# Performance work log

Hardware: AMD Instinct MI355X
Metric: run time of the kernel (lower is better)

Reference implementation:

```python
import jax, jax.numpy as jnp
import numpy as np

IN, H, OUT = 1536, 640, 10
BATCH = 65536
KEEP = 0.1


def setup_inputs() -> dict:
    key = jax.random.key(0)
    kx, k1, k2, k3, m1, m2, m3 = jax.random.split(key, 7)
    # torch.nn.Linear-style weights: (out_features, in_features)
    W1 = jax.random.normal(k1, (H, IN), dtype=jnp.float32) * (1.0 / np.sqrt(IN))
    W2 = jax.random.normal(k2, (H, H), dtype=jnp.float32) * (1.0 / np.sqrt(H))
    W3 = jax.random.normal(k3, (OUT, H), dtype=jnp.float32) * (1.0 / np.sqrt(H))
    return {
        "x": jax.random.normal(kx, (BATCH, IN), dtype=jnp.float32),
        "W1": W1,
        "W2": W2,
        "W3": W3,
        "mask1": jax.random.bernoulli(m1, KEEP, (H, IN)),
        "mask2": jax.random.bernoulli(m2, KEEP, (H, H)),
        "mask3": jax.random.bernoulli(m3, KEEP, (OUT, H)),
    }


def reference(x, W1, W2, W3, mask1, mask2, mask3):
    w1 = jnp.where(mask1, W1, 0.0)
    w2 = jnp.where(mask2, W2, 0.0)
    w3 = jnp.where(mask3, W3, 0.0)
    h = jax.nn.gelu(x @ w1.T, approximate=False)       # [B, 640], exact GELU like F.gelu
    h = jax.nn.gelu(h @ w2.T, approximate=False)       # [B, 640]
    return h @ w3.T                                    # [B, 10]
```

## Files before the change

### kernel.cpp

```cpp
#include <hip/hip_runtime.h>
#include <hip/hip_fp16.h>
#include <math.h>

typedef _Float16 half_t;
typedef __attribute__((ext_vector_type(8))) _Float16 f16x8;
typedef __attribute__((ext_vector_type(4))) float   f32x4;
typedef __attribute__((ext_vector_type(4))) float   float4v;

#define IN_F   1536
#define HID    640
#define OUT_F  10
#define NBATCH 65536

#define SB() __builtin_amdgcn_sched_barrier(0)


__device__ __forceinline__ void gll16(const void* g, const void* l) {
    __builtin_amdgcn_global_load_lds(
        (const __attribute__((address_space(1))) unsigned*)g,
        (__attribute__((address_space(3))) unsigned*)l, 16, 0, 0);
}

__device__ __forceinline__ float gelu_fast(float z) {
    float x  = 0.70710678118654752f * z;
    float ax = fabsf(x);
    float t  = 1.0f / (1.0f + 0.3275911f * ax);
    float p  = t * (0.254829592f +
               t * (-0.284496736f +
               t * (1.421413741f +
               t * (-1.453152027f +
               t * 1.061405429f))));
    float e  = __expf(-ax * ax);
    float er = 1.0f - p * e;
    er = (x < 0.0f) ? -er : er;
    return 0.5f * z * (1.0f + er);
}


__global__ void k_detect(const unsigned* __restrict__ m, int nDwords, int* flags) {
    int f = 0, g = 0;
    for (int i = blockIdx.x * blockDim.x + threadIdx.x; i < nDwords;
         i += gridDim.x * blockDim.x) {
        unsigned d = m[i];
        f |= (d == 0x3F800000u);
        g |= (d != 0u) & (d != 1u) & (d != 0x3F800000u);
    }
    if (f) atomicOr(&flags[0], 1);
    if (g) atomicOr(&flags[1], 1);
}

__device__ __forceinline__ bool mask_at(const void* mask, int i, int isB, int isF) {
    if (isB) return ((const unsigned char*)mask)[i] != 0;
    if (isF) return ((const float*)mask)[i] != 0.0f;
    return ((const int*)mask)[i] != 0;
}

__global__ void k_mask_all(const float* __restrict__ W1, const float* __restrict__ W2,
                           const float* __restrict__ W3,
                           const void* __restrict__ m1, const void* __restrict__ m2,
                           const void* __restrict__ m3,
                           half_t* __restrict__ W1h, half_t* __restrict__ W2h,
                           float* __restrict__ W3m, const int* __restrict__ flags) {
    const int isB = flags[1], isF = flags[0];
    const int N1 = HID * IN_F, N2 = HID * HID, N3 = OUT_F * HID;
    const int NT = N1 + N2 + N3;
    for (int i = blockIdx.x * blockDim.x + threadIdx.x; i < NT;
         i += gridDim.x * blockDim.x) {
        if (i < N1) {
            W1h[i] = mask_at(m1, i, isB, isF) ? (half_t)W1[i] : (half_t)0.0f;
        } else if (i < N1 + N2) {
            int j = i - N1;
            W2h[j] = mask_at(m2, j, isB, isF) ? (half_t)W2[j] : (half_t)0.0f;
        } else {
            int j = i - N1 - N2;
            W3m[j] = mask_at(m3, j, isB, isF) ? W3[j] : 0.0f;
        }
    }
}

__global__ __launch_bounds__(256, 3) void gemm1_tall(
    const float* __restrict__ Ain, const half_t* __restrict__ Bw,
    half_t* __restrict__ Cout) {
    constexpr int K    = IN_F;
    constexpr int NK   = K / 32;
    constexpr int SLAB = 16384 + 10240;
    __shared__ __align__(16) char lds[2 * SLAB];

    const int t = threadIdx.x, lane = t & 63, wid = t >> 6;
    const int wr = wid >> 1, wc = wid & 1;

    const int q       = (int)gridDim.x >> 3;
    const int logical = ((int)blockIdx.x & 7) * q + ((int)blockIdx.x >> 3);
    const int mb = logical >> 2, nbk = logical & 3;
    const long mBase = (long)mb * 128;
    const int  n0    = nbk * 160;

    const int rr = lane & 15, k8 = lane >> 4;

    int aRd[4], bRd[5];
    {
#pragma unroll
        for (int mf = 0; mf < 4; ++mf) {
            const int row = wr * 64 + mf * 16 + rr;
            aRd[mf] = row * 128 + (((2 * k8) ^ (row & 7)) << 4);
        }
#pragma unroll
        for (int nf = 0; nf < 5; ++nf) {
            const int nrow = wc * 80 + nf * 16 + rr, ln = nrow >> 1;
            bRd[nf] = 16384 + ln * 128 +
                      ((((((nrow & 1) << 2) | k8)) ^ (ln & 7)) << 4);
        }
    }

    const float* srcAf;
    {
        const int row = t >> 3, kq = (t & 7) ^ ((t >> 3) & 7);
        srcAf = Ain + (mBase + row) * (long)K + kq * 4;
    }
    const half_t* srcB;
    {
        const int line = t >> 3, orig = (t & 7) ^ (line & 7);
        const int nrow = 2 * line + (orig >> 2), kq = orig & 3;
        srcB = Bw + (size_t)(n0 + nrow) * K + kq * 8;
    }

    auto STAGE = [&](int k, int sb) {
        const size_t ko = (size_t)k * 32;
#pragma unroll
        for (int r = 0; r < 4; ++r)
            gll16(srcAf + ko + (size_t)r * 32 * K,
                  &lds[sb + (t + r * 256) * 16]);
#pragma unroll
        for (int r = 0; r < 2; ++r)
            gll16(srcB + ko + (size_t)r * 64 * K,
                  &lds[sb + 16384 + (t + r * 256) * 16]);
        if (t < 128)
            gll16(srcB + ko + (size_t)128 * K,
                  &lds[sb + 16384 + (t + 512) * 16]);
    };

    f32x4 acc[4][5];
#pragma unroll
    for (int mf = 0; mf < 4; ++mf)
#pragma unroll
        for (int nf = 0; nf < 5; ++nf) {
            f32x4 z = {0.f, 0.f, 0.f, 0.f};
            acc[mf][nf] = z;
        }

    STAGE(0, 0); SB();
    STAGE(1, SLAB); SB();

    for (int ks = 0; ks < NK; ++ks) {
        const int cb = (ks & 1) * SLAB;
        if (ks + 1 < NK) {
            if (wid < 2) asm volatile("s_waitcnt vmcnt(7)" ::: "memory");
            else         asm volatile("s_waitcnt vmcnt(6)" ::: "memory");
        } else {
            asm volatile("s_waitcnt vmcnt(0)" ::: "memory");
        }
        __builtin_amdgcn_s_barrier();
        f16x8 bv[5];
#pragma unroll
        for (int nf = 0; nf < 5; ++nf)
            bv[nf] = *(const f16x8*)(&lds[cb + bRd[nf]]);
        f16x8 av[4];
#pragma unroll
        for (int mf = 0; mf < 4; ++mf) {
            float4v alo = *(const float4v*)(&lds[cb + aRd[mf]]);
            float4v ahi = *(const float4v*)(&lds[cb + (aRd[mf] ^ 16)]);
            f16x8 h;
#pragma unroll
            for (int i = 0; i < 4; ++i) {
                h[i]     = (half_t)alo[i];
                h[i + 4] = (half_t)ahi[i];
            }
            av[mf] = h;
        }
        asm volatile("s_waitcnt lgkmcnt(0)" ::: "memory");
        SB();
        __builtin_amdgcn_s_barrier();
        if (ks + 2 < NK) { STAGE(ks + 2, cb); SB(); }
#pragma unroll
        for (int mf = 0; mf < 4; ++mf)
#pragma unroll
            for (int nf = 0; nf < 5; ++nf)
                acc[mf][nf] = __builtin_amdgcn_mfma_f32_16x16x32_f16(
                    av[mf], bv[nf], acc[mf][nf], 0, 0, 0);
    }

    const int crow0 = (lane >> 4) * 4;
    const int ccol  = lane & 15;
#pragma unroll
    for (int mf = 0; mf < 4; ++mf)
#pragma unroll
        for (int nf = 0; nf < 5; ++nf)
#pragma unroll
            for (int j = 0; j < 4; ++j) {
                const long row = mBase + wr * 64 + mf * 16 + crow0 + j;
                const int  col = n0 + wc * 80 + nf * 16 + ccol;
                Cout[row * HID + col] = (half_t)gelu_fast(acc[mf][nf][j]);
            }
}

template <int K>
__global__ __launch_bounds__(512, 2) void gemm2_fused(
    const half_t* __restrict__ Ain, const half_t* __restrict__ Bw,
    const float* __restrict__ W3, float* __restrict__ Pout) {
    constexpr int NK     = K / 32;
    constexpr int ABYTES = 16384;
    constexpr int SLAB   = ABYTES + 20480;
    __shared__ __align__(16) char lds[3 * SLAB];

    const int t = threadIdx.x, lane = t & 63, wid = t >> 6;
    const int wr = wid >> 2, wc = wid & 3;

    const int q       = (int)gridDim.x >> 3;
    const int logical = ((int)blockIdx.x & 7) * q + ((int)blockIdx.x >> 3);
    const int mb = logical >> 1, nbk = logical & 1;
    const long mBase = (long)mb * 256;
    const int  n0    = nbk * 320;

    const int rr = lane & 15, k8 = lane >> 4;

    int aBase0 = 0, bBase = 0;
    {
        const int row = wr * 128 + rr, ln = row >> 1;
        aBase0 = ln * 128 + ((((((row & 1) << 2) | k8)) ^ (ln & 7)) << 4);
        const int nrow = wc * 80 + rr, lnb = nrow >> 1;
        bBase = ABYTES + lnb * 128 +
                ((((((nrow & 1) << 2) | k8)) ^ (lnb & 7)) << 4);
    }

    const half_t* srcAh;
    {
        const int line = t >> 3, orig = (t & 7) ^ (line & 7);
        const int row = 2 * line + (orig >> 2), kq = orig & 3;
        srcAh = Ain + (mBase + row) * (long)K + kq * 8;
    }
    const half_t* srcB;
    {
        const int line = t >> 3, orig = (t & 7) ^ (line & 7);
        const int nrow = 2 * line + (orig >> 2), kq = orig & 3;
        srcB = Bw + (size_t)(n0 + nrow) * K + kq * 8;
    }

    auto STAGE = [&](int k, int sb) {
        const size_t ko = (size_t)k * 32;
#pragma unroll
        for (int r = 0; r < 2; ++r)
            gll16(srcAh + ko + (size_t)r * 128 * K,
                  &lds[sb + (t + r * 512) * 16]);
#pragma unroll
        for (int r = 0; r < 2; ++r)
            gll16(srcB + ko + (size_t)r * 128 * K,
                  &lds[sb + ABYTES + (t + r * 512) * 16]);
        if (t < 256)
            gll16(srcB + ko + (size_t)2 * 128 * K,
                  &lds[sb + ABYTES + (t + 1024) * 16]);
    };

    f32x4 acc[8][5];
#pragma unroll
    for (int mf = 0; mf < 8; ++mf)
#pragma unroll
        for (int nf = 0; nf < 5; ++nf) {
            f32x4 z = {0.f, 0.f, 0.f, 0.f};
            acc[mf][nf] = z;
        }

    STAGE(0, 0); SB();
    STAGE(1, SLAB); SB();

    for (int ks = 0; ks < NK; ++ks) {
        if (ks + 1 < NK) {
            if (wid < 4) asm volatile("s_waitcnt vmcnt(5)" ::: "memory");
            else         asm volatile("s_waitcnt vmcnt(4)" ::: "memory");
        } else {
            asm volatile("s_waitcnt vmcnt(0)" ::: "memory");
        }
        __builtin_amdgcn_s_barrier();
        const int cb = (ks % 3) * SLAB;
        if (ks + 2 < NK) { STAGE(ks + 2, ((ks + 2) % 3) * SLAB); SB(); }

        f16x8 bv[5];
#pragma unroll
        for (int nf = 0; nf < 5; ++nf)
            bv[nf] = *(const f16x8*)(&lds[cb + bBase + nf * 1024]);
        f16x8 av[8];
#pragma unroll
        for (int mf = 0; mf < 8; ++mf)
            av[mf] = *(const f16x8*)(&lds[cb + aBase0 + mf * 1024]);
#pragma unroll
        for (int mf = 0; mf < 8; ++mf)
#pragma unroll
            for (int nf = 0; nf < 5; ++nf)
                acc[mf][nf] = __builtin_amdgcn_mfma_f32_16x16x32_f16(
                    av[mf], bv[nf], acc[mf][nf], 0, 0, 0);
    }

    const int crow0 = (lane >> 4) * 4;
    const int ccol  = lane & 15;
    float w3[OUT_F][5];
#pragma unroll
    for (int o = 0; o < OUT_F; ++o)
#pragma unroll
        for (int nf = 0; nf < 5; ++nf)
            w3[o][nf] = W3[o * HID + n0 + wc * 80 + nf * 16 + ccol];
    float* slice = Pout + (size_t)(nbk * 4 + wc) * NBATCH * OUT_F;
#pragma unroll
    for (int mf = 0; mf < 8; ++mf)
#pragma unroll
        for (int j = 0; j < 4; ++j) {
            float p[OUT_F];
#pragma unroll
            for (int o = 0; o < OUT_F; ++o) p[o] = 0.f;
#pragma unroll
            for (int nf = 0; nf < 5; ++nf) {
                const float v = gelu_fast(acc[mf][nf][j]);
#pragma unroll
                for (int o = 0; o < OUT_F; ++o) p[o] += v * w3[o][nf];
            }
#pragma unroll
            for (int mask = 1; mask < 16; mask <<= 1)
#pragma unroll
                for (int o = 0; o < OUT_F; ++o)
                    p[o] += __shfl_xor(p[o], mask);
            float v = 0.f;
#pragma unroll
            for (int o = 0; o < OUT_F; ++o) v = (ccol == o) ? p[o] : v;
            const long row = mBase + wr * 128 + mf * 16 + crow0 + j;
            if (ccol < OUT_F) slice[row * OUT_F + ccol] = v;
        }
}

__global__ void k_final(const float* __restrict__ P, float* __restrict__ out) {
    const int n = NBATCH * OUT_F;
    for (int i = blockIdx.x * blockDim.x + threadIdx.x; i < n;
         i += gridDim.x * blockDim.x) {
        float s0 = P[i]                 + P[(size_t)1 * n + i];
        float s1 = P[(size_t)2 * n + i] + P[(size_t)3 * n + i];
        float s2 = P[(size_t)4 * n + i] + P[(size_t)5 * n + i];
        float s3 = P[(size_t)6 * n + i] + P[(size_t)7 * n + i];
        out[i] = (s0 + s1) + (s2 + s3);
    }
}


extern "C" void kernel_launch(void* const* d_in, const int* in_sizes, int n_in,
                              void* d_out, int out_size, void* d_ws, size_t ws_size,
                              hipStream_t stream) {
    const float* x  = (const float*)d_in[0];
    const float* W1 = (const float*)d_in[1];
    const float* W2 = (const float*)d_in[2];
    const float* W3 = (const float*)d_in[3];
    const void*  m1 = d_in[4];
    const void*  m2 = d_in[5];
    const void*  m3 = d_in[6];
    float* out = (float*)d_out;

    char* ws = (char*)d_ws;
    int*    flags = (int*)ws;
    half_t* W1h = (half_t*)(ws + 256);
    half_t* W2h = (half_t*)(ws + 256 + 1966080);
    float*  W3m = (float*)(ws + 256 + 1966080 + 819200);
    half_t* h1  = (half_t*)(ws + 256 + 1966080 + 819200 + 25600);
    float*  Pp  = (float*)((char*)h1 + (size_t)NBATCH * HID * 2);

    hipMemsetAsync(flags, 0, 8, stream);
    k_detect<<<64, 256, 0, stream>>>((const unsigned*)m1, 65536, flags);
    k_mask_all<<<1024, 256, 0, stream>>>(W1, W2, W3, m1, m2, m3, W1h, W2h, W3m, flags);

    gemm1_tall<<<2048, 256, 0, stream>>>(x, W1h, h1);
    gemm2_fused<HID><<<512, 512, 0, stream>>>(h1, W2h, W3m, Pp);
    k_final<<<1024, 256, 0, stream>>>(Pp, out);
}
```

Baseline: 357.3 us.

## Enlarge gemm1 tile to 256x320 with triple-buffered, split-stage LDS pipeline

The first GEMM now uses 512-thread blocks, each computing a 256x320 output tile instead of 128x160. Each fp32 activation row is therefore reloaded only twice across the N dimension instead of four times. The K loop moves to a three-slab LDS ring. Staging of the next-but-one slab is split into two halves, interleaved with the two M-half MFMA phases, and those phases run with raised wave priority via s_setprio. The cost is roughly 156 KB of LDS per block, which allows only one block per CU with fewer resident waves, plus more accumulator registers per thread.

```diff
diff --git a/kernel.cpp b/kernel.cpp
--- a/kernel.cpp
+++ b/kernel.cpp
@@ -78,36 +78,36 @@
     }
 }
 
-__global__ __launch_bounds__(256, 3) void gemm1_tall(
+__global__ __launch_bounds__(512, 2) void gemm1_tall(
     const float* __restrict__ Ain, const half_t* __restrict__ Bw,
     half_t* __restrict__ Cout) {
     constexpr int K    = IN_F;
     constexpr int NK   = K / 32;
-    constexpr int SLAB = 16384 + 10240;
-    __shared__ __align__(16) char lds[2 * SLAB];
+    constexpr int SLAB = 32768 + 20480;
+    __shared__ __align__(16) char lds[3 * SLAB];
 
     const int t = threadIdx.x, lane = t & 63, wid = t >> 6;
-    const int wr = wid >> 1, wc = wid & 1;
+    const int wr = wid >> 2, wc = wid & 3;
 
     const int q       = (int)gridDim.x >> 3;
     const int logical = ((int)blockIdx.x & 7) * q + ((int)blockIdx.x >> 3);
-    const int mb = logical >> 2, nbk = logical & 3;
-    const long mBase = (long)mb * 128;
-    const int  n0    = nbk * 160;
+    const int mb = logical >> 1, nbk = logical & 1;
+    const long mBase = (long)mb * 256;
+    const int  n0    = nbk * 320;
 
     const int rr = lane & 15, k8 = lane >> 4;
 
-    int aRd[4], bRd[5];
-    {
-#pragma unroll
-        for (int mf = 0; mf < 4; ++mf) {
-            const int row = wr * 64 + mf * 16 + rr;
+    int aRd[8], bRd[5];
+    {
+#pragma unroll
+        for (int mf = 0; mf < 8; ++mf) {
+            const int row = wr * 128 + mf * 16 + rr;
             aRd[mf] = row * 128 + (((2 * k8) ^ (row & 7)) << 4);
         }
 #pragma unroll
         for (int nf = 0; nf < 5; ++nf) {
             const int nrow = wc * 80 + nf * 16 + rr, ln = nrow >> 1;
-            bRd[nf] = 16384 + ln * 128 +
+            bRd[nf] = 32768 + ln * 128 +
                       ((((((nrow & 1) << 2) | k8)) ^ (ln & 7)) << 4);
         }
     }
@@ -124,80 +124,124 @@
         srcB = Bw + (size_t)(n0 + nrow) * K + kq * 8;
     }
 
-    auto STAGE = [&](int k, int sb) {
+    auto STAGE_A01 = [&](int k, int sb) {
         const size_t ko = (size_t)k * 32;
-#pragma unroll
-        for (int r = 0; r < 4; ++r)
-            gll16(srcAf + ko + (size_t)r * 32 * K,
-                  &lds[sb + (t + r * 256) * 16]);
-#pragma unroll
-        for (int r = 0; r < 2; ++r)
-            gll16(srcB + ko + (size_t)r * 64 * K,
-                  &lds[sb + 16384 + (t + r * 256) * 16]);
-        if (t < 128)
-            gll16(srcB + ko + (size_t)128 * K,
-                  &lds[sb + 16384 + (t + 512) * 16]);
+        gll16(srcAf + ko, &lds[sb + t * 16]);
+        gll16(srcAf + ko + (size_t)64 * K, &lds[sb + (t + 512) * 16]);
     };
-
-    f32x4 acc[4][5];
-#pragma unroll
-    for (int mf = 0; mf < 4; ++mf)
+    auto STAGE_A23_B = [&](int k, int sb) {
+        const size_t ko = (size_t)k * 32;
+        gll16(srcAf + ko + (size_t)128 * K, &lds[sb + (t + 1024) * 16]);
+        gll16(srcAf + ko + (size_t)192 * K, &lds[sb + (t + 1536) * 16]);
+        gll16(srcB + ko,                    &lds[sb + 32768 + t * 16]);
+        gll16(srcB + ko + (size_t)128 * K,  &lds[sb + 32768 + (t + 512) * 16]);
+        if (t < 256)
+            gll16(srcB + ko + (size_t)256 * K,
+                  &lds[sb + 32768 + (t + 1024) * 16]);
+    };
+
+    f32x4 acc[8][5];
+#pragma unroll
+    for (int mf = 0; mf < 8; ++mf)
 #pragma unroll
         for (int nf = 0; nf < 5; ++nf) {
             f32x4 z = {0.f, 0.f, 0.f, 0.f};
             acc[mf][nf] = z;
         }
 
-    STAGE(0, 0); SB();
-    STAGE(1, SLAB); SB();
+    STAGE_A01(0, 0); STAGE_A23_B(0, 0); SB();
+    STAGE_A01(1, SLAB); STAGE_A23_B(1, SLAB); SB();
 
     for (int ks = 0; ks < NK; ++ks) {
-        const int cb = (ks & 1) * SLAB;
+        const int cb  = (ks % 3) * SLAB;
+        const int nsb = ((ks + 2) % 3) * SLAB;
+        const bool st = (ks + 2) < NK;
         if (ks + 1 < NK) {
-            if (wid < 2) asm volatile("s_waitcnt vmcnt(7)" ::: "memory");
+            if (wid < 4) asm volatile("s_waitcnt vmcnt(7)" ::: "memory");
             else         asm volatile("s_waitcnt vmcnt(6)" ::: "memory");
         } else {
             asm volatile("s_waitcnt vmcnt(0)" ::: "memory");
         }
         __builtin_amdgcn_s_barrier();
         f16x8 bv[5];
-#pragma unroll
-        for (int nf = 0; nf < 5; ++nf)
-            bv[nf] = *(const f16x8*)(&lds[cb + bRd[nf]]);
-        f16x8 av[4];
-#pragma unroll
-        for (int mf = 0; mf < 4; ++mf) {
-            float4v alo = *(const float4v*)(&lds[cb + aRd[mf]]);
-            float4v ahi = *(const float4v*)(&lds[cb + (aRd[mf] ^ 16)]);
-            f16x8 h;
-#pragma unroll
-            for (int i = 0; i < 4; ++i) {
-                h[i]     = (half_t)alo[i];
-                h[i + 4] = (half_t)ahi[i];
-            }
-            av[mf] = h;
-        }
-        asm volatile("s_waitcnt lgkmcnt(0)" ::: "memory");
-        SB();
-        __builtin_amdgcn_s_barrier();
-        if (ks + 2 < NK) { STAGE(ks + 2, cb); SB(); }
-#pragma unroll
-        for (int mf = 0; mf < 4; ++mf)
+        {
+            float4v alo[4], ahi[4];
+#pragma unroll
+            for (int m2 = 0; m2 < 4; ++m2) {
+                alo[m2] = *(const float4v*)(&lds[cb + aRd[m2]]);
+                ahi[m2] = *(const float4v*)(&lds[cb + (aRd[m2] ^ 16)]);
+            }
 #pragma unroll
             for (int nf = 0; nf < 5; ++nf)
-                acc[mf][nf] = __builtin_amdgcn_mfma_f32_16x16x32_f16(
-                    av[mf], bv[nf], acc[mf][nf], 0, 0, 0);
+                bv[nf] = *(const f16x8*)(&lds[cb + bRd[nf]]);
+            if (st) STAGE_A01(ks + 2, nsb);
+            SB();
+            asm volatile("s_waitcnt lgkmcnt(0)" ::: "memory");
+            SB();
+            f16x8 av[4];
+#pragma unroll
+            for (int m2 = 0; m2 < 4; ++m2) {
+                f16x8 h;
+#pragma unroll
+                for (int i = 0; i < 4; ++i) {
+                    h[i]     = (half_t)alo[m2][i];
+                    h[i + 4] = (half_t)ahi[m2][i];
+                }
+                av[m2] = h;
+            }
+            __builtin_amdgcn_s_setprio(1);
+#pragma unroll
+            for (int m2 = 0; m2 < 4; ++m2)
+#pragma unroll
+                for (int nf = 0; nf < 5; ++nf)
+                    acc[m2][nf] = __builtin_amdgcn_mfma_f32_16x16x32_f16(
+                        av[m2], bv[nf], acc[m2][nf], 0, 0, 0);
+            __builtin_amdgcn_s_setprio(0);
+            SB();
+        }
+        {
+            float4v alo[4], ahi[4];
+#pragma unroll
+            for (int m2 = 0; m2 < 4; ++m2) {
+                alo[m2] = *(const float4v*)(&lds[cb + aRd[4 + m2]]);
+                ahi[m2] = *(const float4v*)(&lds[cb + (aRd[4 + m2] ^ 16)]);
+            }
+            if (st) STAGE_A23_B(ks + 2, nsb);
+            SB();
+            asm volatile("s_waitcnt lgkmcnt(0)" ::: "memory");
+            SB();
+            f16x8 av[4];
+#pragma unroll
+            for (int m2 = 0; m2 < 4; ++m2) {
+                f16x8 h;
+#pragma unroll
+                for (int i = 0; i < 4; ++i) {
+                    h[i]     = (half_t)alo[m2][i];
+                    h[i + 4] = (half_t)ahi[m2][i];
+                }
+                av[m2] = h;
+            }
+            __builtin_amdgcn_s_setprio(1);
+#pragma unroll
+            for (int m2 = 0; m2 < 4; ++m2)
+#pragma unroll
+                for (int nf = 0; nf < 5; ++nf)
+                    acc[4 + m2][nf] = __builtin_amdgcn_mfma_f32_16x16x32_f16(
+                        av[m2], bv[nf], acc[4 + m2][nf], 0, 0, 0);
+            __builtin_amdgcn_s_setprio(0);
+            SB();
+        }
     }
 
     const int crow0 = (lane >> 4) * 4;
     const int ccol  = lane & 15;
 #pragma unroll
-    for (int mf = 0; mf < 4; ++mf)
+    for (int mf = 0; mf < 8; ++mf)
 #pragma unroll
         for (int nf = 0; nf < 5; ++nf)
 #pragma unroll
             for (int j = 0; j < 4; ++j) {
-                const long row = mBase + wr * 64 + mf * 16 + crow0 + j;
+                const long row = mBase + wr * 128 + mf * 16 + crow0 + j;
                 const int  col = n0 + wc * 80 + nf * 16 + ccol;
                 Cout[row * HID + col] = (half_t)gelu_fast(acc[mf][nf][j]);
             }
@@ -371,7 +415,7 @@
     k_detect<<<64, 256, 0, stream>>>((const unsigned*)m1, 65536, flags);
     k_mask_all<<<1024, 256, 0, stream>>>(W1, W2, W3, m1, m2, m3, W1h, W2h, W3m, flags);
 
-    gemm1_tall<<<2048, 256, 0, stream>>>(x, W1h, h1);
+    gemm1_tall<<<512, 512, 0, stream>>>(x, W1h, h1);
     gemm2_fused<HID><<<512, 512, 0, stream>>>(h1, W2h, W3m, Pp);
     k_final<<<1024, 256, 0, stream>>>(Pp, out);
 }
```

Measured after the change: 317.5 us. 11.1% less time.
